# Kernel optimization log

Measured on AMD Instinct MI355X. Metric: run time of the kernel, lower is better.

## Reference

```python
import jax, jax.numpy as jnp
import numpy as np

ALPHA = 0.5
NOISE_KEY = jax.random.key(42)  # fixed key: deterministic stand-in for torch.randn


def setup_inputs() -> dict:
    key = jax.random.key(0)
    k1, k2 = jax.random.split(key)
    N, D, E = 8192, 1024, 131072
    x = jax.random.normal(k1, (N, D), dtype=jnp.float32)
    edge_index = jax.random.randint(k2, (2, E), 0, N, dtype=jnp.int64)
    return {"x": x, "edge_index": edge_index}


def reference(x, edge_index):
    # edge_index is accepted but unused, matching the original module.
    N = x.shape[0]
    m = jax.random.normal(NOISE_KEY, (N, N), dtype=x.dtype)  # [N, N] noise
    M = jax.nn.softmax(m / ALPHA, axis=1)                    # row-wise Gibbs weights
    return M @ x                                             # [N, D]
```

## Files before the change

kernel.cpp:

```cpp
#include <hip/hip_runtime.h>
#include <stdint.h>
#include <stddef.h>

#define NROWS 8192
#define NCOLS 8192
#define DDIM  1024

typedef float  f32x4 __attribute__((ext_vector_type(4)));
typedef _Float16 f16x8 __attribute__((ext_vector_type(8)));

#if __has_builtin(__builtin_amdgcn_exp2f)
#define EXP2F(x) __builtin_amdgcn_exp2f(x)
#else
#define EXP2F(x) exp2f(x)
#endif
#if __has_builtin(__builtin_amdgcn_logf)
#define LOG2F(x) __builtin_amdgcn_logf(x)
#else
#define LOG2F(x) log2f(x)
#endif
#if __has_builtin(__builtin_amdgcn_sqrtf)
#define SQRTF(x) __builtin_amdgcn_sqrtf(x)
#else
#define SQRTF(x) sqrtf(x)
#endif

__device__ __forceinline__ uint32_t rotl32(uint32_t x, uint32_t r){
  return (x << r) | (x >> (32u - r));
}

__device__ __forceinline__ void threefry2x32(uint32_t x0, uint32_t x1,
                                             uint32_t& o0, uint32_t& o1){
  const uint32_t k0 = 0u, k1 = 42u;
  const uint32_t k2 = k0 ^ k1 ^ 0x1BD11BDAu;
  x0 += k0; x1 += k1;
#define TF_R(r) { x0 += x1; x1 = rotl32(x1, r); x1 ^= x0; }
  TF_R(13) TF_R(15) TF_R(26) TF_R(6)
  x0 += k1; x1 += k2 + 1u;
  TF_R(17) TF_R(29) TF_R(16) TF_R(24)
  x0 += k2; x1 += k0 + 2u;
  TF_R(13) TF_R(15) TF_R(26) TF_R(6)
  x0 += k0; x1 += k1 + 3u;
  TF_R(17) TF_R(29) TF_R(16) TF_R(24)
  x0 += k1; x1 += k2 + 4u;
  TF_R(13) TF_R(15) TF_R(26) TF_R(6)
  x0 += k2; x1 += k0 + 5u;
#undef TF_R
  o0 = x0; o1 = x1;
}

__device__ __forceinline__ float elemE(uint32_t f){
  uint32_t o0, o1;
  threefry2x32(0u, f, o0, o1);
  const uint32_t b = o0 ^ o1;
  float u = __uint_as_float((b >> 9) | 0x3F800000u) - 1.0f;
  const float lo = -0.99999994f;
  float v = fmaf(u, 2.0f, lo);
  v = fmaxf(v, lo);
  const float t1 = fmaf(-v, v, 1.0f);
  float w = LOG2F(t1) * (-0.69314718f);
  float p;
  if (w < 5.0f){
    w -= 2.5f;
    p =              3.97426473e-08f;
    p = fmaf(p, w,   4.85465e-07f);
    p = fmaf(p, w,  -4.98283e-06f);
    p = fmaf(p, w,  -6.21053e-06f);
    p = fmaf(p, w,   3.09120e-04f);
    p = fmaf(p, w,  -1.77290e-03f);
    p = fmaf(p, w,  -5.90817e-03f);
    p = fmaf(p, w,   3.48803163e-01f);
    p = fmaf(p, w,   2.12331355e+00f);
  } else {
    w = SQRTF(w) - 3.0f;
    p =             -2.83147363e-04f;
    p = fmaf(p, w,   1.42765560e-04f);
    p = fmaf(p, w,   1.90825981e-03f);
    p = fmaf(p, w,  -5.19500608e-03f);
    p = fmaf(p, w,   8.11688602e-03f);
    p = fmaf(p, w,  -1.07798386e-02f);
    p = fmaf(p, w,   1.33487061e-02f);
    p = fmaf(p, w,   1.41658096e+00f);
    p = fmaf(p, w,   4.00643396e+00f);
  }
  const float m = p * v;
  return EXP2F(fmaf(m, 2.8853900817779268f, -4.0f));
}

__device__ __forceinline__ uint16_t f2h(float a){
  union { _Float16 h; uint16_t u; } c; c.h = (_Float16)a; return c.u;
}

__global__ __launch_bounds__(256) void transpose_cast(const float* __restrict__ x,
                                                      uint16_t* __restrict__ xT){
  __shared__ float tile[32][33];
  const int tx = threadIdx.x & 31;
  const int ty = threadIdx.x >> 5;
  const int dcol = blockIdx.x * 32;
  const int nrow = blockIdx.y * 32;
  #pragma unroll
  for (int r = 0; r < 32; r += 8)
    tile[ty + r][tx] = x[(size_t)(nrow + ty + r) * DDIM + dcol + tx];
  __syncthreads();
  #pragma unroll
  for (int r = 0; r < 32; r += 8)
    xT[(size_t)(dcol + ty + r) * NROWS + nrow + tx] = f2h(tile[tx][ty + r]);
}

__global__ __launch_bounds__(256) void gen_trans_rows(const float* __restrict__ x,
                                                      uint16_t* __restrict__ xT,
                                                      uint16_t* __restrict__ P,
                                                      float* __restrict__ S){
  const int t = threadIdx.x;
  {
    __shared__ float tile[32][33];
    const int tx = t & 31;
    const int ty = t >> 5;
    const int dcol = (blockIdx.x & 31) * 32;
    const int nrow = (blockIdx.x >> 5) * 32;
    #pragma unroll
    for (int r = 0; r < 32; r += 8)
      tile[ty + r][tx] = x[(size_t)(nrow + ty + r) * DDIM + dcol + tx];
    __syncthreads();
    #pragma unroll
    for (int r = 0; r < 32; r += 8)
      xT[(size_t)(dcol + ty + r) * NROWS + nrow + tx] = f2h(tile[tx][ty + r]);
  }
  const int gi = blockIdx.x;
  const uint32_t base = (uint32_t)gi * 8192u;
  uint16_t* __restrict__ prow = P + (size_t)gi * NCOLS;
  float acc = 0.0f;
  #pragma unroll
  for (int g = 0; g < 4; ++g){
    const uint32_t j0 = (uint32_t)(g * 2048) + ((uint32_t)t << 3);
    float e[8];
    #pragma unroll
    for (int i = 0; i < 8; ++i){ e[i] = elemE(base + j0 + (uint32_t)i); acc += e[i]; }
    f16x8 pk;
    #pragma unroll
    for (int i = 0; i < 8; ++i) pk[i] = (_Float16)e[i];
    *reinterpret_cast<f16x8*>(prow + j0) = pk;
  }
  #pragma unroll
  for (int off = 32; off > 0; off >>= 1) acc += __shfl_down(acc, off, 64);
  __shared__ float sm[4];
  __syncthreads();
  if ((t & 63) == 0) sm[t >> 6] = acc;
  __syncthreads();
  if (t == 0) S[gi] = (sm[0] + sm[1]) + (sm[2] + sm[3]);
}

__global__ __launch_bounds__(256) void gen_rows(uint16_t* __restrict__ P,
                                                float* __restrict__ S, int row0){
  const int gi = row0 + blockIdx.x;
  const uint32_t base = (uint32_t)gi * 8192u;
  const int t = threadIdx.x;
  uint16_t* __restrict__ prow = P + (size_t)blockIdx.x * NCOLS;
  float acc = 0.0f;
  #pragma unroll
  for (int g = 0; g < 4; ++g){
    const uint32_t j0 = (uint32_t)(g * 2048) + ((uint32_t)t << 3);
    float e[8];
    #pragma unroll
    for (int i = 0; i < 8; ++i){ e[i] = elemE(base + j0 + (uint32_t)i); acc += e[i]; }
    f16x8 pk;
    #pragma unroll
    for (int i = 0; i < 8; ++i) pk[i] = (_Float16)e[i];
    *reinterpret_cast<f16x8*>(prow + j0) = pk;
  }
  #pragma unroll
  for (int off = 32; off > 0; off >>= 1) acc += __shfl_down(acc, off, 64);
  __shared__ float sm[4];
  if ((t & 63) == 0) sm[t >> 6] = acc;
  __syncthreads();
  if (t == 0) S[gi] = (sm[0] + sm[1]) + (sm[2] + sm[3]);
}

#define BM 128
#define BN 128
#define BK 64

typedef const __attribute__((address_space(1))) void GAS;
typedef __attribute__((address_space(3))) void LAS;

__device__ __forceinline__ void gload16(const void* g, void* l){
  __builtin_amdgcn_global_load_lds((GAS*)g, (LAS*)l, 16, 0, 0);
}

__global__ __launch_bounds__(256, 3) void gemm_rows(
    const uint16_t* __restrict__ P,
    const uint16_t* __restrict__ xT,
    const float* __restrict__ S,
    int row0,
    float* __restrict__ O)
{
  __shared__ uint16_t smem[16384];
  uint16_t* As = smem;
  uint16_t* Bs = smem + 8192;

  const int tid  = threadIdx.x;
  const int lane = tid & 63;
  const int wave = tid >> 6;
  const int wr = (wave >> 1) * 64;
  const int wc = (wave & 1) * 64;
  const int l15 = lane & 15;
  const int lq  = lane >> 4;

  const size_t m0 = (size_t)blockIdx.x * BM;
  const size_t n0 = (size_t)blockIdx.y * BN;

  const int srow = tid >> 3;
  const int sx   = (tid & 7) ^ (srow & 7);
  const uint16_t* gA = P  + (m0 + srow) * (size_t)NCOLS + sx * 8;
  const uint16_t* gB = xT + (n0 + srow) * (size_t)NCOLS + sx * 8;

  f32x4 acc[4][4];
  #pragma unroll
  for (int i = 0; i < 4; ++i)
    #pragma unroll
    for (int j = 0; j < 4; ++j)
      #pragma unroll
      for (int q = 0; q < 4; ++q) acc[i][j][q] = 0.0f;

  const int axor = l15 & 7;

  for (int k0 = 0; k0 < NCOLS; k0 += BK){
    #pragma unroll
    for (int r = 0; r < 4; ++r)
      gload16(gA + (size_t)(32 * r) * NCOLS + k0, As + (tid + 256 * r) * 8);
    #pragma unroll
    for (int r = 0; r < 4; ++r)
      gload16(gB + (size_t)(32 * r) * NCOLS + k0, Bs + (tid + 256 * r) * 8);
    __syncthreads();
    #pragma unroll
    for (int ks = 0; ks < 2; ++ks){
      const int kphys = ((lq + 4 * ks) ^ axor) * 8;
      f16x8 af[4], bfrag[4];
      #pragma unroll
      for (int i = 0; i < 4; ++i)
        af[i] = *reinterpret_cast<const f16x8*>(As + (wr + i*16 + l15) * BK + kphys);
      #pragma unroll
      for (int j = 0; j < 4; ++j)
        bfrag[j] = *reinterpret_cast<const f16x8*>(Bs + (wc + j*16 + l15) * BK + kphys);
      #pragma unroll
      for (int i = 0; i < 4; ++i)
        #pragma unroll
        for (int j = 0; j < 4; ++j)
          acc[i][j] = __builtin_amdgcn_mfma_f32_16x16x32_f16(af[i], bfrag[j], acc[i][j], 0, 0, 0);
    }
    __syncthreads();
  }

  #pragma unroll
  for (int i = 0; i < 4; ++i){
    float rinv[4];
    #pragma unroll
    for (int r = 0; r < 4; ++r)
      rinv[r] = 1.0f / S[row0 + m0 + wr + i*16 + lq*4 + r];
    #pragma unroll
    for (int j = 0; j < 4; ++j){
      const size_t col = n0 + wc + j*16 + l15;
      #pragma unroll
      for (int r = 0; r < 4; ++r){
        const size_t row = m0 + wr + i*16 + lq*4 + r;
        O[row * DDIM + col] = acc[i][j][r] * rinv[r];
      }
    }
  }
}

extern "C" void kernel_launch(void* const* d_in, const int* in_sizes, int n_in,
                              void* d_out, int out_size, void* d_ws, size_t ws_size,
                              hipStream_t stream)
{
  (void)in_sizes; (void)n_in; (void)out_size;
  const float* x = (const float*)d_in[0];
  float* O = (float*)d_out;
  uint8_t* ws = (uint8_t*)d_ws;

  float* S = (float*)ws;
  const size_t S_bytes = (size_t)NROWS * sizeof(float);
  uint16_t* xT = (uint16_t*)(ws + S_bytes);
  const size_t xT_bytes = (size_t)DDIM * NROWS * sizeof(uint16_t);
  uint16_t* P = (uint16_t*)(ws + S_bytes + xT_bytes);
  const size_t used = S_bytes + xT_bytes;
  const size_t avail = ws_size > used ? ws_size - used : 0;

  const size_t fullP = (size_t)NROWS * NCOLS * sizeof(uint16_t);
  if (avail >= fullP){
    gen_trans_rows<<<NROWS, 256, 0, stream>>>(x, xT, P, S);
    gemm_rows<<<dim3(NROWS/BM, DDIM/BN), 256, 0, stream>>>(P, xT, S, 0, O);
  } else {
    transpose_cast<<<dim3(DDIM/32, NROWS/32), 256, 0, stream>>>(x, xT);
    int R = 128;
    for (int r = 4096; r >= 128; r >>= 1)
      if ((size_t)r * NCOLS * sizeof(uint16_t) <= avail){ R = r; break; }
    for (int r0 = 0; r0 < NROWS; r0 += R){
      gen_rows<<<R, 256, 0, stream>>>(P, S, r0);
      gemm_rows<<<dim3(R/BM, DDIM/BN), 256, 0, stream>>>(P, xT, S, r0, O + (size_t)r0 * DDIM);
    }
  }
}
```

Baseline: 325.7 us.

## Add 256x128-tile triple-buffered GEMM kernel with block swizzle for full-P path

Replaces the 128x128 GEMM on the full-workspace path with a new 512-thread kernel using 256x128 tiles. It triple-buffers LDS via direct global-to-LDS loads with a two-stage prefetch, raises MFMA priority, and remaps block ids so neighbouring blocks share A or B tiles in cache. The aim is to hide load latency and cut global reads of P per output. In exchange it uses 144KB of dynamic LDS and heavy register use, and the launch does not raise the dynamic shared memory limit, which may restrict occupancy or cause launch failure.

After: 353.2 us. 1.08x slower.

```diff
diff --git a/kernel.cpp b/kernel.cpp
--- a/kernel.cpp
+++ b/kernel.cpp
@@ -176,16 +176,16 @@
   if (t == 0) S[gi] = (sm[0] + sm[1]) + (sm[2] + sm[3]);
 }
 
+typedef const __attribute__((address_space(1))) void GAS;
+typedef __attribute__((address_space(3))) void LAS;
+
+__device__ __forceinline__ void gload16(const void* g, void* l){
+  __builtin_amdgcn_global_load_lds((GAS*)g, (LAS*)l, 16, 0, 0);
+}
+
 #define BM 128
 #define BN 128
 #define BK 64
-
-typedef const __attribute__((address_space(1))) void GAS;
-typedef __attribute__((address_space(3))) void LAS;
-
-__device__ __forceinline__ void gload16(const void* g, void* l){
-  __builtin_amdgcn_global_load_lds((GAS*)g, (LAS*)l, 16, 0, 0);
-}
 
 __global__ __launch_bounds__(256, 3) void gemm_rows(
     const uint16_t* __restrict__ P,
@@ -269,6 +269,117 @@
   }
 }
 
+#define GM 256
+#define GN 128
+#define GK 64
+#define GNT (NCOLS / GK)
+#define GBUF 24576
+
+__global__ __launch_bounds__(512, 2) void gemm256(
+    const uint16_t* __restrict__ P,
+    const uint16_t* __restrict__ xT,
+    const float* __restrict__ S,
+    float* __restrict__ O)
+{
+  extern __shared__ uint16_t sm[];
+
+  const int tid  = threadIdx.x;
+  const int lane = tid & 63;
+  const int wave = tid >> 6;
+  const int wr = (wave >> 1) * 64;
+  const int wc = (wave & 1) * 64;
+  const int l15 = lane & 15;
+  const int lq  = lane >> 4;
+  const int axor = l15 & 7;
+
+  const int b   = blockIdx.x;
+  const int swz = (b & 7) * 32 + (b >> 3);
+  const size_t m0 = (size_t)(swz & 31) * GM;
+  const size_t n0 = (size_t)(swz >> 5) * GN;
+
+  const int srow = tid >> 3;
+  const int sx   = (tid & 7) ^ (srow & 7);
+  const uint16_t* gA = P  + (m0 + srow) * (size_t)NCOLS + sx * 8;
+  const uint16_t* gB = xT + (n0 + srow) * (size_t)NCOLS + sx * 8;
+
+  uint16_t* buf0 = sm;
+  uint16_t* buf1 = sm + GBUF;
+  uint16_t* buf2 = sm + 2 * GBUF;
+
+  auto STAGE = [&](uint16_t* base, int kt){
+    const int kk = kt * GK;
+    #pragma unroll
+    for (int r = 0; r < 4; ++r)
+      gload16(gA + (size_t)(64 * r) * NCOLS + kk, base + (tid + 512 * r) * 8);
+    #pragma unroll
+    for (int r = 0; r < 2; ++r)
+      gload16(gB + (size_t)(64 * r) * NCOLS + kk, base + 16384 + (tid + 512 * r) * 8);
+  };
+
+  f32x4 acc[4][4];
+  #pragma unroll
+  for (int i = 0; i < 4; ++i)
+    #pragma unroll
+    for (int j = 0; j < 4; ++j)
+      #pragma unroll
+      for (int q = 0; q < 4; ++q) acc[i][j][q] = 0.0f;
+
+  STAGE(buf0, 0);
+  STAGE(buf1, 1);
+  asm volatile("s_waitcnt vmcnt(6)" ::: "memory");
+  __builtin_amdgcn_s_barrier();
+
+  uint16_t *pc = buf0, *pn = buf1, *ps = buf2;
+  for (int t = 0; t < GNT; ++t){
+    if (t + 2 < GNT) STAGE(ps, t + 2);
+
+    f16x8 af[2][4], bf[2][4];
+    #pragma unroll
+    for (int ks = 0; ks < 2; ++ks){
+      const int kphys = ((lq + 4 * ks) ^ axor) * 8;
+      #pragma unroll
+      for (int i = 0; i < 4; ++i)
+        af[ks][i] = *reinterpret_cast<const f16x8*>(pc + (wr + i*16 + l15) * GK + kphys);
+      #pragma unroll
+      for (int j = 0; j < 4; ++j)
+        bf[ks][j] = *reinterpret_cast<const f16x8*>(pc + 16384 + (wc + j*16 + l15) * GK + kphys);
+    }
+
+    __builtin_amdgcn_s_setprio(1);
+    #pragma unroll
+    for (int ks = 0; ks < 2; ++ks)
+      #pragma unroll
+      for (int i = 0; i < 4; ++i)
+        #pragma unroll
+        for (int j = 0; j < 4; ++j)
+          acc[i][j] = __builtin_amdgcn_mfma_f32_16x16x32_f16(af[ks][i], bf[ks][j], acc[i][j], 0, 0, 0);
+    __builtin_amdgcn_s_setprio(0);
+
+    if (t + 2 < GNT) asm volatile("s_waitcnt vmcnt(6) lgkmcnt(0)" ::: "memory");
+    else             asm volatile("s_waitcnt vmcnt(0) lgkmcnt(0)" ::: "memory");
+    __builtin_amdgcn_s_barrier();
+
+    uint16_t* tmp = pc; pc = pn; pn = ps; ps = tmp;
+  }
+
+  #pragma unroll
+  for (int i = 0; i < 4; ++i){
+    float rinv[4];
+    #pragma unroll
+    for (int r = 0; r < 4; ++r)
+      rinv[r] = 1.0f / S[m0 + wr + i*16 + lq*4 + r];
+    #pragma unroll
+    for (int j = 0; j < 4; ++j){
+      const size_t col = n0 + wc + j*16 + l15;
+      #pragma unroll
+      for (int r = 0; r < 4; ++r){
+        const size_t row = m0 + wr + i*16 + lq*4 + r;
+        O[row * DDIM + col] = acc[i][j][r] * rinv[r];
+      }
+    }
+  }
+}
+
 extern "C" void kernel_launch(void* const* d_in, const int* in_sizes, int n_in,
                               void* d_out, int out_size, void* d_ws, size_t ws_size,
                               hipStream_t stream)
@@ -289,7 +400,7 @@
   const size_t fullP = (size_t)NROWS * NCOLS * sizeof(uint16_t);
   if (avail >= fullP){
     gen_trans_rows<<<NROWS, 256, 0, stream>>>(x, xT, P, S);
-    gemm_rows<<<dim3(NROWS/BM, DDIM/BN), 256, 0, stream>>>(P, xT, S, 0, O);
+    gemm256<<<dim3(256), 512, 3 * GBUF * sizeof(uint16_t), stream>>>(P, xT, S, O);
   } else {
     transpose_cast<<<dim3(DDIM/32, NROWS/32), 256, 0, stream>>>(x, xT);
     int R = 128;
```

## Fuse noise generation and softmax weights into GEMM, dropping the materialized P matrix

Applied to the files above, without the earlier changes.

Removes the separate kernel that wrote the full 8192x8192 fp16 weight matrix P plus the row sums, along with the GEMM that read P back. A single fused kernel now generates the A tile on the fly in LDS for each K step, double-buffers the B tile (the transposed x) via global_load_lds, and reduces the row sums in-kernel before normalizing the output. Each block covers 32 rows and the full 1024-wide D, so B is streamed once per block across 256 blocks. The cost is recomputing the noise inside the GEMM loop, a per-step full barrier, and low block count with large LDS use (about 132 KB per block).

Measured after the change: 479.6 us. 1.47x slower.

```diff
diff --git a/kernel.cpp b/kernel.cpp
--- a/kernel.cpp
+++ b/kernel.cpp
@@ -107,79 +107,6 @@
     xT[(size_t)(dcol + ty + r) * NROWS + nrow + tx] = f2h(tile[tx][ty + r]);
 }
 
-__global__ __launch_bounds__(256) void gen_trans_rows(const float* __restrict__ x,
-                                                      uint16_t* __restrict__ xT,
-                                                      uint16_t* __restrict__ P,
-                                                      float* __restrict__ S){
-  const int t = threadIdx.x;
-  {
-    __shared__ float tile[32][33];
-    const int tx = t & 31;
-    const int ty = t >> 5;
-    const int dcol = (blockIdx.x & 31) * 32;
-    const int nrow = (blockIdx.x >> 5) * 32;
-    #pragma unroll
-    for (int r = 0; r < 32; r += 8)
-      tile[ty + r][tx] = x[(size_t)(nrow + ty + r) * DDIM + dcol + tx];
-    __syncthreads();
-    #pragma unroll
-    for (int r = 0; r < 32; r += 8)
-      xT[(size_t)(dcol + ty + r) * NROWS + nrow + tx] = f2h(tile[tx][ty + r]);
-  }
-  const int gi = blockIdx.x;
-  const uint32_t base = (uint32_t)gi * 8192u;
-  uint16_t* __restrict__ prow = P + (size_t)gi * NCOLS;
-  float acc = 0.0f;
-  #pragma unroll
-  for (int g = 0; g < 4; ++g){
-    const uint32_t j0 = (uint32_t)(g * 2048) + ((uint32_t)t << 3);
-    float e[8];
-    #pragma unroll
-    for (int i = 0; i < 8; ++i){ e[i] = elemE(base + j0 + (uint32_t)i); acc += e[i]; }
-    f16x8 pk;
-    #pragma unroll
-    for (int i = 0; i < 8; ++i) pk[i] = (_Float16)e[i];
-    *reinterpret_cast<f16x8*>(prow + j0) = pk;
-  }
-  #pragma unroll
-  for (int off = 32; off > 0; off >>= 1) acc += __shfl_down(acc, off, 64);
-  __shared__ float sm[4];
-  __syncthreads();
-  if ((t & 63) == 0) sm[t >> 6] = acc;
-  __syncthreads();
-  if (t == 0) S[gi] = (sm[0] + sm[1]) + (sm[2] + sm[3]);
-}
-
-__global__ __launch_bounds__(256) void gen_rows(uint16_t* __restrict__ P,
-                                                float* __restrict__ S, int row0){
-  const int gi = row0 + blockIdx.x;
-  const uint32_t base = (uint32_t)gi * 8192u;
-  const int t = threadIdx.x;
-  uint16_t* __restrict__ prow = P + (size_t)blockIdx.x * NCOLS;
-  float acc = 0.0f;
-  #pragma unroll
-  for (int g = 0; g < 4; ++g){
-    const uint32_t j0 = (uint32_t)(g * 2048) + ((uint32_t)t << 3);
-    float e[8];
-    #pragma unroll
-    for (int i = 0; i < 8; ++i){ e[i] = elemE(base + j0 + (uint32_t)i); acc += e[i]; }
-    f16x8 pk;
-    #pragma unroll
-    for (int i = 0; i < 8; ++i) pk[i] = (_Float16)e[i];
-    *reinterpret_cast<f16x8*>(prow + j0) = pk;
-  }
-  #pragma unroll
-  for (int off = 32; off > 0; off >>= 1) acc += __shfl_down(acc, off, 64);
-  __shared__ float sm[4];
-  if ((t & 63) == 0) sm[t >> 6] = acc;
-  __syncthreads();
-  if (t == 0) S[gi] = (sm[0] + sm[1]) + (sm[2] + sm[3]);
-}
-
-#define BM 128
-#define BN 128
-#define BK 64
-
 typedef const __attribute__((address_space(1))) void GAS;
 typedef __attribute__((address_space(3))) void LAS;
 
@@ -187,84 +114,112 @@
   __builtin_amdgcn_global_load_lds((GAS*)g, (LAS*)l, 16, 0, 0);
 }
 
-__global__ __launch_bounds__(256, 3) void gemm_rows(
-    const uint16_t* __restrict__ P,
+#define FM2 32
+#define FK2 32
+#define NST (NCOLS / FK2)
+#define LB0 0
+#define LB1 32768
+#define LA0 65536
+#define LA1 66560
+#define LDS_ELEMS 67584
+
+__global__ __launch_bounds__(512, 2) void fused32(
     const uint16_t* __restrict__ xT,
-    const float* __restrict__ S,
-    int row0,
     float* __restrict__ O)
 {
-  __shared__ uint16_t smem[16384];
-  uint16_t* As = smem;
-  uint16_t* Bs = smem + 8192;
-
-  const int tid  = threadIdx.x;
-  const int lane = tid & 63;
-  const int wave = tid >> 6;
-  const int wr = (wave >> 1) * 64;
-  const int wc = (wave & 1) * 64;
-  const int l15 = lane & 15;
-  const int lq  = lane >> 4;
-
-  const size_t m0 = (size_t)blockIdx.x * BM;
-  const size_t n0 = (size_t)blockIdx.y * BN;
-
-  const int srow = tid >> 3;
-  const int sx   = (tid & 7) ^ (srow & 7);
-  const uint16_t* gA = P  + (m0 + srow) * (size_t)NCOLS + sx * 8;
-  const uint16_t* gB = xT + (n0 + srow) * (size_t)NCOLS + sx * 8;
-
-  f32x4 acc[4][4];
-  #pragma unroll
-  for (int i = 0; i < 4; ++i)
-    #pragma unroll
-    for (int j = 0; j < 4; ++j)
-      #pragma unroll
-      for (int q = 0; q < 4; ++q) acc[i][j][q] = 0.0f;
-
-  const int axor = l15 & 7;
-
-  for (int k0 = 0; k0 < NCOLS; k0 += BK){
-    #pragma unroll
-    for (int r = 0; r < 4; ++r)
-      gload16(gA + (size_t)(32 * r) * NCOLS + k0, As + (tid + 256 * r) * 8);
-    #pragma unroll
-    for (int r = 0; r < 4; ++r)
-      gload16(gB + (size_t)(32 * r) * NCOLS + k0, Bs + (tid + 256 * r) * 8);
-    __syncthreads();
-    #pragma unroll
-    for (int ks = 0; ks < 2; ++ks){
-      const int kphys = ((lq + 4 * ks) ^ axor) * 8;
-      f16x8 af[4], bfrag[4];
-      #pragma unroll
-      for (int i = 0; i < 4; ++i)
-        af[i] = *reinterpret_cast<const f16x8*>(As + (wr + i*16 + l15) * BK + kphys);
-      #pragma unroll
-      for (int j = 0; j < 4; ++j)
-        bfrag[j] = *reinterpret_cast<const f16x8*>(Bs + (wc + j*16 + l15) * BK + kphys);
-      #pragma unroll
-      for (int i = 0; i < 4; ++i)
-        #pragma unroll
-        for (int j = 0; j < 4; ++j)
-          acc[i][j] = __builtin_amdgcn_mfma_f32_16x16x32_f16(af[i], bfrag[j], acc[i][j], 0, 0, 0);
+  extern __shared__ uint16_t sm[];
+
+  const int t = threadIdx.x;
+  const size_t m0 = (size_t)blockIdx.x * FM2;
+
+  const int lane = t & 63;
+  const int w    = t >> 6;
+  const int wr   = (w >> 2) * 16;
+  const int wn0  = (w & 3) * 256;
+  const int l15  = lane & 15;
+  const int lq   = lane >> 4;
+  const int kb   = (lq ^ (l15 & 3)) * 8;
+
+  const int grow = t >> 4;
+  const int gq   = t & 15;
+  const uint32_t genbase = (uint32_t)(m0 + (size_t)grow) * 8192u + (uint32_t)(gq * 2);
+  const int aoff = grow * FK2 + (((gq >> 2) ^ (grow & 3)) * 8) + (gq & 3) * 2;
+
+  const int srow = t >> 2;
+  const int sg   = (t & 3) ^ (srow & 3);
+  const uint16_t* gB = xT + (size_t)srow * NCOLS + sg * 8;
+
+  float myS = 0.0f;
+  f32x4 acc[16];
+  #pragma unroll
+  for (int n = 0; n < 16; ++n)
+    #pragma unroll
+    for (int r = 0; r < 4; ++r) acc[n][r] = 0.0f;
+
+  auto STAGEB = [&](int lb, int s){
+    const int k0 = s * FK2;
+    #pragma unroll
+    for (int r = 0; r < 8; ++r)
+      gload16(gB + (size_t)(128 * r) * NCOLS + k0, sm + lb + (t + 512 * r) * 8);
+  };
+  auto GENA = [&](int la, int s){
+    const uint32_t f0 = genbase + (uint32_t)(s * FK2);
+    float e0 = elemE(f0);
+    float e1 = elemE(f0 + 1u);
+    myS += e0 + e1;
+    union { _Float16 h[2]; uint32_t u; } pk;
+    pk.h[0] = (_Float16)e0; pk.h[1] = (_Float16)e1;
+    *reinterpret_cast<uint32_t*>(sm + la + aoff) = pk.u;
+  };
+
+  auto STEP = [&](int lb, int la, int lb2, int la2, int s){
+    if (s + 1 < NST){
+      STAGEB(lb2, s + 1);
+      GENA(la2, s + 1);
     }
-    __syncthreads();
+    const f16x8 af = *reinterpret_cast<const f16x8*>(sm + la + (wr + l15) * FK2 + kb);
+    __builtin_amdgcn_s_setprio(1);
+    #pragma unroll
+    for (int n = 0; n < 16; ++n){
+      const f16x8 bf = *reinterpret_cast<const f16x8*>(sm + lb + (wn0 + n * 16 + l15) * FK2 + kb);
+      acc[n] = __builtin_amdgcn_mfma_f32_16x16x32_f16(af, bf, acc[n], 0, 0, 0);
+    }
+    __builtin_amdgcn_s_setprio(0);
+    asm volatile("s_waitcnt vmcnt(0) lgkmcnt(0)" ::: "memory");
+    __builtin_amdgcn_s_barrier();
+  };
+
+  STAGEB(LB0, 0);
+  GENA(LA0, 0);
+  asm volatile("s_waitcnt vmcnt(0) lgkmcnt(0)" ::: "memory");
+  __builtin_amdgcn_s_barrier();
+
+  for (int s2 = 0; s2 < NST; s2 += 2){
+    STEP(LB0, LA0, LB1, LA1, s2);
+    STEP(LB1, LA1, LB0, LA0, s2 + 1);
   }
 
-  #pragma unroll
-  for (int i = 0; i < 4; ++i){
-    float rinv[4];
-    #pragma unroll
-    for (int r = 0; r < 4; ++r)
-      rinv[r] = 1.0f / S[row0 + m0 + wr + i*16 + lq*4 + r];
-    #pragma unroll
-    for (int j = 0; j < 4; ++j){
-      const size_t col = n0 + wc + j*16 + l15;
-      #pragma unroll
-      for (int r = 0; r < 4; ++r){
-        const size_t row = m0 + wr + i*16 + lq*4 + r;
-        O[row * DDIM + col] = acc[i][j][r] * rinv[r];
-      }
+  float v = myS;
+  v += __shfl_down(v, 8, 16);
+  v += __shfl_down(v, 4, 16);
+  v += __shfl_down(v, 2, 16);
+  v += __shfl_down(v, 1, 16);
+  float* Ssum = reinterpret_cast<float*>(sm);
+  if (l15 == 0) Ssum[w * 4 + lq] = v;
+  __syncthreads();
+
+  float rinv[4];
+  #pragma unroll
+  for (int r = 0; r < 4; ++r)
+    rinv[r] = 1.0f / Ssum[wr + lq * 4 + r];
+
+  #pragma unroll
+  for (int n = 0; n < 16; ++n){
+    const size_t col = (size_t)wn0 + n * 16 + l15;
+    #pragma unroll
+    for (int r = 0; r < 4; ++r){
+      const size_t row = m0 + wr + lq * 4 + r;
+      __builtin_nontemporal_store(acc[n][r] * rinv[r], &O[row * DDIM + col]);
     }
   }
 }
@@ -278,26 +233,10 @@
   float* O = (float*)d_out;
   uint8_t* ws = (uint8_t*)d_ws;
 
-  float* S = (float*)ws;
-  const size_t S_bytes = (size_t)NROWS * sizeof(float);
-  uint16_t* xT = (uint16_t*)(ws + S_bytes);
+  uint16_t* xT = (uint16_t*)ws;
   const size_t xT_bytes = (size_t)DDIM * NROWS * sizeof(uint16_t);
-  uint16_t* P = (uint16_t*)(ws + S_bytes + xT_bytes);
-  const size_t used = S_bytes + xT_bytes;
-  const size_t avail = ws_size > used ? ws_size - used : 0;
-
-  const size_t fullP = (size_t)NROWS * NCOLS * sizeof(uint16_t);
-  if (avail >= fullP){
-    gen_trans_rows<<<NROWS, 256, 0, stream>>>(x, xT, P, S);
-    gemm_rows<<<dim3(NROWS/BM, DDIM/BN), 256, 0, stream>>>(P, xT, S, 0, O);
-  } else {
-    transpose_cast<<<dim3(DDIM/32, NROWS/32), 256, 0, stream>>>(x, xT);
-    int R = 128;
-    for (int r = 4096; r >= 128; r >>= 1)
-      if ((size_t)r * NCOLS * sizeof(uint16_t) <= avail){ R = r; break; }
-    for (int r0 = 0; r0 < NROWS; r0 += R){
-      gen_rows<<<R, 256, 0, stream>>>(P, S, r0);
-      gemm_rows<<<dim3(R/BM, DDIM/BN), 256, 0, stream>>>(P, xT, S, r0, O + (size_t)r0 * DDIM);
-    }
-  }
-}
+  if (ws_size < xT_bytes) return;
+
+  transpose_cast<<<dim3(DDIM/32, NROWS/32), 256, 0, stream>>>(x, xT);
+  fused32<<<256, 512, LDS_ELEMS * sizeof(uint16_t), stream>>>(xT, O);
+}
```
